# Kernel tuning notes

Measured on AMD Instinct MI355X. Metric: run time of the kernel, lower is better.

## Reference

```python
import jax, jax.numpy as jnp
import numpy as np

D_MODEL = 1024
D_FF = 4096


def _layernorm(x, g, b, eps=1e-5):
    mu = jnp.mean(x, axis=-1, keepdims=True)
    var = jnp.var(x, axis=-1, keepdims=True)
    return (x - mu) * jax.lax.rsqrt(var + eps) * g + b


def setup_inputs() -> dict:
    key = jax.random.key(0)
    ks = jax.random.split(key, 16)
    d, f = D_MODEL, D_FF
    s = 1.0 / np.sqrt(d)
    inp = {
        'x': jax.random.normal(ks[0], (4, 2048, d), dtype=jnp.float32),
        'wq': jax.random.uniform(ks[1], (d, d), jnp.float32, -s, s),
        'bq': jax.random.uniform(ks[2], (d,), jnp.float32, -s, s),
        'wk': jax.random.uniform(ks[3], (d, d), jnp.float32, -s, s),
        'bk': jax.random.uniform(ks[4], (d,), jnp.float32, -s, s),
        'wv': jax.random.uniform(ks[5], (d, d), jnp.float32, -s, s),
        'bv': jax.random.uniform(ks[6], (d,), jnp.float32, -s, s),
        'wo': jax.random.uniform(ks[7], (d, d), jnp.float32, -s, s),
        'bo': jax.random.uniform(ks[8], (d,), jnp.float32, -s, s),
        'w1': jax.random.uniform(ks[9], (d, f), jnp.float32, -s, s),
        'b1': jax.random.uniform(ks[10], (f,), jnp.float32, -s, s),
        'w2': jax.random.uniform(ks[11], (f, d), jnp.float32, -1.0 / np.sqrt(f), 1.0 / np.sqrt(f)),
        'b2': jax.random.uniform(ks[12], (d,), jnp.float32, -1.0 / np.sqrt(f), 1.0 / np.sqrt(f)),
        'g1': jnp.ones((d,), jnp.float32),
        'be1': jnp.zeros((d,), jnp.float32),
        'g2': jnp.ones((d,), jnp.float32),
        'be2': jnp.zeros((d,), jnp.float32),
    }
    return inp


def reference(x, wq, bq, wk, bk, wv, bv, wo, bo, w1, b1, w2, b2, g1, be1, g2, be2):
    d_k = x.shape[-1]
    q = jnp.einsum('bsd,de->bse', x, wq) + bq
    k = jnp.einsum('bsd,de->bse', x, wk) + bk
    v = jnp.einsum('bsd,de->bse', x, wv) + bv
    # full-width attention (no head split in the original module)
    scores = jnp.einsum('bqd,bkd->bqk', q, k) / jnp.sqrt(jnp.float32(d_k))
    attn = jax.nn.softmax(scores, axis=-1)
    ctx = jnp.einsum('bqk,bkd->bqd', attn, v)
    attn_out = jnp.einsum('bsd,de->bse', ctx, wo) + bo
    x1 = _layernorm(x + attn_out, g1, be1)
    ff = jnp.einsum('bsf,fd->bsd', jax.nn.relu(jnp.einsum('bsd,df->bsf', x1, w1) + b1), w2) + b2
    return _layernorm(x1 + ff, g2, be2)
```

## Files before the change

kernel.cpp:

```cpp
#include <hip/hip_runtime.h>
#include <stdint.h>


using f32x4 = __attribute__((ext_vector_type(4))) float;
using s16x8 = __attribute__((ext_vector_type(8))) short;

__device__ __forceinline__ ushort f2b(float f) {
    union { float f; uint32_t u; } v; v.f = f;
    uint32_t u = v.u;
    return (ushort)((u + 0x7fffu + ((u >> 16) & 1u)) >> 16);
}
__device__ __forceinline__ float b2f(ushort b) {
    union { uint32_t u; float f; } v; v.u = ((uint32_t)b) << 16;
    return v.f;
}
__device__ __forceinline__ float to_f(float f) { return f; }
__device__ __forceinline__ float to_f(ushort b) { return b2f(b); }

__device__ __forceinline__ void async_ld16(const ushort* g, ushort* l) {
    __builtin_amdgcn_global_load_lds(
        (const __attribute__((address_space(1))) void*)g,
        (__attribute__((address_space(3))) void*)l,
        16, 0, 0);
}

#define WAITCNT_VM4 0x0F74
#define WAITCNT_VM0 0x0F70


__global__ __launch_bounds__(256) void cast_f2b4(const float* __restrict__ src,
                                                 ushort* __restrict__ dst,
                                                 long long n4) {
    long long i = (long long)blockIdx.x * 256 + threadIdx.x;
    if (i >= n4) return;
    float4 f = ((const float4*)src)[i];
    ushort4 o;
    o.x = f2b(f.x); o.y = f2b(f.y); o.z = f2b(f.z); o.w = f2b(f.w);
    ((ushort4*)dst)[i] = o;
}


__global__ __launch_bounds__(256) void concat3(const float* __restrict__ a,
                                               const float* __restrict__ b,
                                               const float* __restrict__ c,
                                               float* __restrict__ dst) {
    int i = blockIdx.x * 256 + threadIdx.x;
    const float* s = (i < 1024) ? a : (i < 2048) ? b : c;
    dst[i] = s[i & 1023];
}


template <typename T>
__global__ __launch_bounds__(256) void transpose_to_bf16(const T* __restrict__ src,
                                                         ushort* __restrict__ dst,
                                                         int R, int C, int srcLd,
                                                         long long ss, long long ds) {
    __shared__ float tile[32][33];
    src += (long long)blockIdx.z * ss;
    dst += (long long)blockIdx.z * ds;
    const int c0 = blockIdx.x * 32;
    const int r0 = blockIdx.y * 32;
    const int tx = threadIdx.x, ty = threadIdx.y;
#pragma unroll
    for (int i = 0; i < 4; i++) {
        int r = r0 + ty + i * 8;
        tile[ty + i * 8][tx] = to_f(src[(long long)r * srcLd + c0 + tx]);
    }
    __syncthreads();
#pragma unroll
    for (int i = 0; i < 4; i++) {
        int r = c0 + ty + i * 8;
        dst[(long long)r * R + r0 + tx] = f2b(tile[tx][ty + i * 8]);
    }
}


__global__ __launch_bounds__(256) void transpose4_to_bf16(const float* __restrict__ s0,
                                                          const float* __restrict__ s1,
                                                          const float* __restrict__ s2,
                                                          const float* __restrict__ s3,
                                                          ushort* __restrict__ dst) {
    __shared__ float tile[32][33];
    const int D = 1024;
    const int z = blockIdx.z;
    const float* src = (z == 0) ? s0 : (z == 1) ? s1 : (z == 2) ? s2 : s3;
    dst += (long long)z * D * D;
    const int c0 = blockIdx.x * 32;
    const int r0 = blockIdx.y * 32;
    const int tx = threadIdx.x, ty = threadIdx.y;
#pragma unroll
    for (int i = 0; i < 4; i++) {
        int r = r0 + ty + i * 8;
        tile[ty + i * 8][tx] = src[(long long)r * D + c0 + tx];
    }
    __syncthreads();
#pragma unroll
    for (int i = 0; i < 4; i++) {
        int r = c0 + ty + i * 8;
        dst[(long long)r * D + r0 + tx] = f2b(tile[tx][ty + i * 8]);
    }
}


#define BM 128
#define BN 128
#define BKK 32
#define TILE_ELEMS (BM * BKK)

template <int OUT_BF16, int RELU, int HAS_BIAS>
__global__ __launch_bounds__(256, 4) void gemm_bt(const ushort* __restrict__ A,
                                                  const ushort* __restrict__ BT,
                                                  void* __restrict__ Cp,
                                                  const float* __restrict__ bias,
                                                  int N, int K, int kChunks, float scale,
                                                  int lda, int ldb, int ldc,
                                                  long long sA, long long sB, long long sC,
                                                  long long sK) {
    __shared__ ushort As[2 * TILE_ELEMS];
    __shared__ ushort Bs[2 * TILE_ELEMS];

    const int tid = threadIdx.x;
    const int kIdx = blockIdx.z % kChunks;
    const int bz = blockIdx.z / kChunks;
    const int kLen = K / kChunks;
    const int kOff = kIdx * kLen;
    const ushort* Ab = A + (long long)bz * sA;
    const ushort* Bb = BT + (long long)bz * sB;

    const int W = gridDim.x, H = gridDim.y;
    const int b = blockIdx.y * W + blockIdx.x;
    const int Hp = H >> 3;
    const int xcd = b & 7;
    const int s = b >> 3;
    const int tn = s / Hp;
    const int tm = xcd * Hp + (s % Hp);

    const int lane = tid & 63;
    const int wave = tid >> 6;
    const int wm = (wave >> 1) * 64;
    const int wn = (wave & 1) * 64;
    const int quad = lane >> 4;
    const int l16 = lane & 15;

    const int srow = wave * 32 + (lane >> 2);
    const int scol = (lane & 3) * 8;
    const ushort* AgL = Ab + (long long)(tm * BM + srow) * lda + scol + kOff;
    const ushort* BgL = Bb + (long long)(tn * BN + srow) * ldb + scol + kOff;
    ushort* AsL = As + wave * 1024;
    ushort* BsL = Bs + wave * 1024;
    const long long rstepA = (long long)16 * lda;
    const long long rstepB = (long long)16 * ldb;

    f32x4 acc[4][4];
#pragma unroll
    for (int i = 0; i < 4; i++)
#pragma unroll
        for (int j = 0; j < 4; j++) acc[i][j] = (f32x4){0.f, 0.f, 0.f, 0.f};

    async_ld16(AgL, AsL);
    async_ld16(AgL + rstepA, AsL + 512);
    async_ld16(BgL, BsL);
    async_ld16(BgL + rstepB, BsL + 512);

    int p = 0;
    for (int k0 = 0; k0 < kLen; k0 += BKK) {
        if (k0 + BKK < kLen) {
            const int q = p ^ 1;
            async_ld16(AgL + (k0 + BKK), AsL + q * TILE_ELEMS);
            async_ld16(AgL + rstepA + (k0 + BKK), AsL + q * TILE_ELEMS + 512);
            async_ld16(BgL + (k0 + BKK), BsL + q * TILE_ELEMS);
            async_ld16(BgL + rstepB + (k0 + BKK), BsL + q * TILE_ELEMS + 512);
            __builtin_amdgcn_s_waitcnt(WAITCNT_VM4);
        } else {
            __builtin_amdgcn_s_waitcnt(WAITCNT_VM0);
        }
        __builtin_amdgcn_s_barrier();

        const ushort* Asp = As + p * TILE_ELEMS;
        const ushort* Bsp = Bs + p * TILE_ELEMS;
        s16x8 af[4], bf[4];
#pragma unroll
        for (int i = 0; i < 4; i++)
            af[i] = *(const s16x8*)&Asp[(wm + i * 16 + l16) * BKK + quad * 8];
#pragma unroll
        for (int j = 0; j < 4; j++)
            bf[j] = *(const s16x8*)&Bsp[(wn + j * 16 + l16) * BKK + quad * 8];
#pragma unroll
        for (int i = 0; i < 4; i++)
#pragma unroll
            for (int j = 0; j < 4; j++)
                acc[i][j] = __builtin_amdgcn_mfma_f32_16x16x32_bf16(af[i], bf[j], acc[i][j], 0, 0, 0);

        __builtin_amdgcn_s_barrier();
        p ^= 1;
    }

    const long long cb = (long long)bz * sC + (long long)kIdx * sK;
    float* Cf = (float*)Cp;
    ushort* Cb = (ushort*)Cp;
#pragma unroll
    for (int j = 0; j < 4; j++) {
        const int col = tn * BN + wn + j * 16 + l16;
        float bv = (HAS_BIAS && kIdx == 0) ? bias[col] : 0.0f;
#pragma unroll
        for (int i = 0; i < 4; i++) {
            const int row0 = tm * BM + wm + i * 16 + quad * 4;
#pragma unroll
            for (int r = 0; r < 4; r++) {
                float v = acc[i][j][r] * scale + bv;
                if (RELU) v = v > 0.f ? v : 0.f;
                long long idx = cb + (long long)(row0 + r) * ldc + col;
                if (OUT_BF16) Cb[idx] = f2b(v);
                else Cf[idx] = v;
            }
        }
    }
}


__global__ __launch_bounds__(256) void softmax_rows(const ushort* __restrict__ S,
                                                    ushort* __restrict__ P) {
    const int C = 2048;
    const long long row = blockIdx.x;
    const int tid = threadIdx.x;
    const ushort4* s4 = (const ushort4*)(S + row * C) + tid * 2;
    ushort4 a = s4[0], bq = s4[1];
    float v[8];
    v[0] = b2f(a.x); v[1] = b2f(a.y); v[2] = b2f(a.z); v[3] = b2f(a.w);
    v[4] = b2f(bq.x); v[5] = b2f(bq.y); v[6] = b2f(bq.z); v[7] = b2f(bq.w);
    float mx = -1e30f;
#pragma unroll
    for (int i = 0; i < 8; i++) mx = fmaxf(mx, v[i]);
    __shared__ float red[256];
    red[tid] = mx;
    __syncthreads();
    for (int off = 128; off > 0; off >>= 1) {
        if (tid < off) red[tid] = fmaxf(red[tid], red[tid + off]);
        __syncthreads();
    }
    mx = red[0];
    __syncthreads();
    float sum = 0.f;
#pragma unroll
    for (int i = 0; i < 8; i++) {
        v[i] = __expf(v[i] - mx);
        sum += v[i];
    }
    red[tid] = sum;
    __syncthreads();
    for (int off = 128; off > 0; off >>= 1) {
        if (tid < off) red[tid] += red[tid + off];
        __syncthreads();
    }
    float inv = 1.f / red[0];
    ushort4 o0, o1;
    o0.x = f2b(v[0] * inv); o0.y = f2b(v[1] * inv); o0.z = f2b(v[2] * inv); o0.w = f2b(v[3] * inv);
    o1.x = f2b(v[4] * inv); o1.y = f2b(v[5] * inv); o1.z = f2b(v[6] * inv); o1.w = f2b(v[7] * inv);
    ushort4* p4 = (ushort4*)(P + row * C) + tid * 2;
    p4[0] = o0;
    p4[1] = o1;
}


__global__ __launch_bounds__(256) void residual_ln(const float* __restrict__ X,
                                                   const float* __restrict__ Y,
                                                   const float* __restrict__ Y2,
                                                   const float* __restrict__ g,
                                                   const float* __restrict__ be,
                                                   float* __restrict__ outf,
                                                   ushort* __restrict__ outb) {
    const int D = 1024;
    const long long row = blockIdx.x;
    const float* x = X + row * D;
    const float* y = Y + row * D;
    const float* y2 = Y2 ? Y2 + row * D : nullptr;
    const int tid = threadIdx.x;
    float v[4];
    float s = 0.f, s2 = 0.f;
#pragma unroll
    for (int i = 0; i < 4; i++) {
        int c = tid + i * 256;
        float t = x[c] + y[c];
        if (y2) t += y2[c];
        v[i] = t;
        s += t;
        s2 += t * t;
    }
    __shared__ float r1[256], r2[256];
    r1[tid] = s;
    r2[tid] = s2;
    __syncthreads();
    for (int off = 128; off > 0; off >>= 1) {
        if (tid < off) {
            r1[tid] += r1[tid + off];
            r2[tid] += r2[tid + off];
        }
        __syncthreads();
    }
    float mu = r1[0] * (1.f / 1024.f);
    float var = r2[0] * (1.f / 1024.f) - mu * mu;
    float inv = rsqrtf(var + 1e-5f);
    float* of = outf + row * D;
    ushort* ob = outb ? outb + row * D : nullptr;
#pragma unroll
    for (int i = 0; i < 4; i++) {
        int c = tid + i * 256;
        float o = (v[i] - mu) * inv * g[c] + be[c];
        of[c] = o;
        if (ob) ob[c] = f2b(o);
    }
}


extern "C" void kernel_launch(void* const* d_in, const int* in_sizes, int n_in,
                              void* d_out, int out_size, void* d_ws, size_t ws_size,
                              hipStream_t stream) {
    const float* x  = (const float*)d_in[0];
    const float* wq = (const float*)d_in[1];
    const float* bq = (const float*)d_in[2];
    const float* wk = (const float*)d_in[3];
    const float* bk = (const float*)d_in[4];
    const float* wv = (const float*)d_in[5];
    const float* bv = (const float*)d_in[6];
    const float* wo = (const float*)d_in[7];
    const float* bo = (const float*)d_in[8];
    const float* w1 = (const float*)d_in[9];
    const float* b1 = (const float*)d_in[10];
    const float* w2 = (const float*)d_in[11];
    const float* b2 = (const float*)d_in[12];
    const float* g1 = (const float*)d_in[13];
    const float* be1 = (const float*)d_in[14];
    const float* g2 = (const float*)d_in[15];
    const float* be2 = (const float*)d_in[16];
    float* out = (float*)d_out;
    char* ws = (char*)d_ws;

    const int Bz = 4, S = 2048, D = 1024, F = 4096;
    const int T = Bz * S;
    const size_t MBy = 1024ull * 1024ull;

    ushort* qkvT = (ushort*)(ws + 0);
    ushort* woT  = (ushort*)(ws + 6 * MBy);
    ushort* w1T  = (ushort*)(ws + 8 * MBy);
    ushort* w2T  = (ushort*)(ws + 16 * MBy);
    float*  bqkv = (float*)(ws + 24 * MBy);
    ushort* xb   = (ushort*)(ws + 25 * MBy);
    ushort* qkv  = (ushort*)(ws + 41 * MBy);
    ushort* vT   = (ushort*)(ws + 89 * MBy);
    ushort* scb  = (ushort*)(ws + 105 * MBy);
    ushort* attn = (ushort*)(ws + 169 * MBy);
    ushort* ctx = (ushort*)(ws + 25 * MBy);
    float*  ao0 = (float*)(ws + 105 * MBy);
    float*  ao1 = (float*)(ws + 137 * MBy);
    float*  x1  = (float*)(ws + 41 * MBy);
    ushort* x1b = (ushort*)(ws + 73 * MBy);
    ushort* h   = (ushort*)(ws + 105 * MBy);
    float*  ff0 = (float*)(ws + 169 * MBy);
    float*  ff1 = (float*)(ws + 73 * MBy);

    dim3 b32(32, 8);

    cast_f2b4<<<(T * D) / 1024, 256, 0, stream>>>(x, xb, (long long)(T * D) / 4);

    transpose4_to_bf16<<<dim3(32, 32, 4), b32, 0, stream>>>(wq, wk, wv, wo, qkvT);
    transpose_to_bf16<float><<<dim3(128, 32, 1), b32, 0, stream>>>(w1, w1T, D, F, F, 0, 0);
    transpose_to_bf16<float><<<dim3(32, 128, 1), b32, 0, stream>>>(w2, w2T, F, D, D, 0, 0);

    concat3<<<12, 256, 0, stream>>>(bq, bk, bv, bqkv);

    gemm_bt<1, 0, 1><<<dim3(3 * D / 128, T / 128, 1), 256, 0, stream>>>(
        xb, qkvT, qkv, bqkv, 3 * D, D, 1, 1.f, D, D, 3 * D, 0, 0, 0, 0);

    transpose_to_bf16<ushort><<<dim3(D / 32, S / 32, Bz), b32, 0, stream>>>(
        qkv + 2048, vT, S, D, 3 * D, (long long)S * 3 * D, (long long)S * D);

    gemm_bt<1, 0, 0><<<dim3(S / 128, S / 128, Bz), 256, 0, stream>>>(
        qkv, qkv + 1024, scb, nullptr, S, D, 1, 0.03125f, 3 * D, 3 * D, S,
        (long long)S * 3 * D, (long long)S * 3 * D, (long long)S * S, 0);

    softmax_rows<<<T, 256, 0, stream>>>(scb, attn);

    gemm_bt<1, 0, 0><<<dim3(D / 128, S / 128, Bz), 256, 0, stream>>>(
        attn, vT, ctx, nullptr, D, S, 1, 1.f, S, S, D,
        (long long)S * S, (long long)D * S, (long long)S * D, 0);

    gemm_bt<0, 0, 1><<<dim3(D / 128, T / 128, 2), 256, 0, stream>>>(
        ctx, woT, ao0, bo, D, D, 2, 1.f, D, D, D, 0, 0, 0, (long long)(ao1 - ao0));

    residual_ln<<<T, 256, 0, stream>>>(x, ao0, ao1, g1, be1, x1, x1b);

    gemm_bt<1, 1, 1><<<dim3(F / 128, T / 128, 1), 256, 0, stream>>>(
        x1b, w1T, h, b1, F, D, 1, 1.f, D, D, F, 0, 0, 0, 0);

    gemm_bt<0, 0, 1><<<dim3(D / 128, T / 128, 2), 256, 0, stream>>>(
        h, w2T, ff0, b2, D, F, 2, 1.f, F, F, D, 0, 0, 0, (long long)(ff1 - ff0));

    residual_ln<<<T, 256, 0, stream>>>(x1, ff0, ff1, g2, be2, out, nullptr);
}
```

Before: 596.0 us.

## Replace 128x128 GEMM with 256x256 8-wave swizzled pipelined GEMM kernel

Replaces the 128x128x32 bf16 MFMA GEMM with a 256x256x64 tile kernel using 512 threads. It uses XOR-swizzled LDS layouts, a staged half-tile async prefetch interleaved with four MFMA phases, and s_setprio around the MFMA blocks. The larger tile raises arithmetic intensity and cuts global traffic per flop. The attention-times-V GEMM is now split-K into two fp32 partials, followed by a new add-and-cast kernel that produces bf16 ctx. The costs are lower occupancy, fewer blocks on small grids (for example 4x8x8), and an extra pass over memory for ctx.

```diff
diff --git a/kernel.cpp b/kernel.cpp
--- a/kernel.cpp
+++ b/kernel.cpp
@@ -24,8 +24,9 @@
         16, 0, 0);
 }
 
-#define WAITCNT_VM4 0x0F74
-#define WAITCNT_VM0 0x0F70
+#define WAITCNT_VM6   0x0F76
+#define WAITCNT_VM0   0x0F70
+#define WAITCNT_LGKM0 0xC07F
 
 
 __global__ __launch_bounds__(256) void cast_f2b4(const float* __restrict__ src,
@@ -47,6 +48,21 @@
     int i = blockIdx.x * 256 + threadIdx.x;
     const float* s = (i < 1024) ? a : (i < 2048) ? b : c;
     dst[i] = s[i & 1023];
+}
+
+
+__global__ __launch_bounds__(256) void add2_cast(const float* __restrict__ a,
+                                                 const float* __restrict__ b,
+                                                 ushort* __restrict__ o,
+                                                 long long n4) {
+    long long i = (long long)blockIdx.x * 256 + threadIdx.x;
+    if (i >= n4) return;
+    float4 x = ((const float4*)a)[i];
+    float4 y = ((const float4*)b)[i];
+    ushort4 u;
+    u.x = f2b(x.x + y.x); u.y = f2b(x.y + y.y);
+    u.z = f2b(x.z + y.z); u.w = f2b(x.w + y.w);
+    ((ushort4*)o)[i] = u;
 }
 
 
@@ -102,109 +118,168 @@
 }
 
 
-#define BM 128
-#define BN 128
-#define BKK 32
-#define TILE_ELEMS (BM * BKK)
-
 template <int OUT_BF16, int RELU, int HAS_BIAS>
-__global__ __launch_bounds__(256, 4) void gemm_bt(const ushort* __restrict__ A,
+__global__ __launch_bounds__(512, 2) void gemm256(const ushort* __restrict__ A,
                                                   const ushort* __restrict__ BT,
                                                   void* __restrict__ Cp,
                                                   const float* __restrict__ bias,
-                                                  int N, int K, int kChunks, float scale,
+                                                  int K, int kChunks, float scale,
                                                   int lda, int ldb, int ldc,
-                                                  long long sA, long long sB, long long sC,
-                                                  long long sK) {
-    __shared__ ushort As[2 * TILE_ELEMS];
-    __shared__ ushort Bs[2 * TILE_ELEMS];
+                                                  long long sA, long long sB,
+                                                  long long sC, long long sK) {
+    __shared__ ushort Asl[32768];
+    __shared__ ushort Bsl[32768];
 
     const int tid = threadIdx.x;
     const int kIdx = blockIdx.z % kChunks;
     const int bz = blockIdx.z / kChunks;
     const int kLen = K / kChunks;
     const int kOff = kIdx * kLen;
+    const int kTiles = kLen >> 6;
     const ushort* Ab = A + (long long)bz * sA;
     const ushort* Bb = BT + (long long)bz * sB;
 
     const int W = gridDim.x, H = gridDim.y;
-    const int b = blockIdx.y * W + blockIdx.x;
+    const int bidx = blockIdx.y * W + blockIdx.x;
     const int Hp = H >> 3;
-    const int xcd = b & 7;
-    const int s = b >> 3;
-    const int tn = s / Hp;
-    const int tm = xcd * Hp + (s % Hp);
+    const int xcd = bidx & 7;
+    const int sb = bidx >> 3;
+    const int tn = sb / Hp;
+    const int tm = xcd * Hp + sb % Hp;
 
     const int lane = tid & 63;
-    const int wave = tid >> 6;
-    const int wm = (wave >> 1) * 64;
-    const int wn = (wave & 1) * 64;
+    const int w = tid >> 6;
+    const int wm = w >> 2;
+    const int wn = w & 3;
+    const int l16 = lane & 15;
     const int quad = lane >> 4;
-    const int l16 = lane & 15;
-
-    const int srow = wave * 32 + (lane >> 2);
-    const int scol = (lane & 3) * 8;
-    const ushort* AgL = Ab + (long long)(tm * BM + srow) * lda + scol + kOff;
-    const ushort* BgL = Bb + (long long)(tn * BN + srow) * ldb + scol + kOff;
-    ushort* AsL = As + wave * 1024;
-    ushort* BsL = Bs + wave * 1024;
-    const long long rstepA = (long long)16 * lda;
-    const long long rstepB = (long long)16 * ldb;
-
-    f32x4 acc[4][4];
-#pragma unroll
-    for (int i = 0; i < 4; i++)
+
+    const int lr = lane >> 3;
+    const int swslot = (lane & 7) ^ lr;
+    const ushort* AgS = Ab + (long long)(tm * 256 + w * 16 + lr) * lda + kOff + swslot * 8;
+    const ushort* BgS = Bb + (long long)(tn * 256 + w * 16 + lr) * ldb + kOff + swslot * 8;
+    ushort* AsW = Asl + w * 1024;
+    ushort* BsW = Bsl + w * 1024;
+
+#define STG_A(h, tt, bf) { const ushort* g_ = AgS + (h) * 128 * lda + (tt) * 64;   \
+        ushort* d_ = AsW + (bf) * 16384 + (h) * 8192;                              \
+        async_ld16(g_, d_); async_ld16(g_ + 8 * lda, d_ + 512); }
+#define STG_B(h, tt, bf) { const ushort* g_ = BgS + (h) * 128 * ldb + (tt) * 64;   \
+        ushort* d_ = BsW + (bf) * 16384 + (h) * 8192;                              \
+        async_ld16(g_, d_); async_ld16(g_ + 8 * ldb, d_ + 512); }
+
+    const int csw0 = (quad * 8) ^ ((l16 & 7) * 8);
+    const int csw1 = (32 + quad * 8) ^ ((l16 & 7) * 8);
+    const int aoff0 = l16 * 64 + csw0;
+    const int aoff1 = l16 * 64 + csw1;
+    const ushort* AhB = Asl + wm * 8192;
+    const ushort* BhB = Bsl + (wn >> 1) * 8192 + (wn & 1) * 4096;
+
+    f32x4 acc[8][4];
+#pragma unroll
+    for (int i = 0; i < 8; i++)
 #pragma unroll
         for (int j = 0; j < 4; j++) acc[i][j] = (f32x4){0.f, 0.f, 0.f, 0.f};
 
-    async_ld16(AgL, AsL);
-    async_ld16(AgL + rstepA, AsL + 512);
-    async_ld16(BgL, BsL);
-    async_ld16(BgL + rstepB, BsL + 512);
+    STG_B(0, 0, 0); STG_A(0, 0, 0); STG_B(1, 0, 0); STG_A(1, 0, 0);
+    STG_B(0, 1, 1); STG_A(0, 1, 1); STG_B(1, 1, 1);
+    __builtin_amdgcn_s_waitcnt(WAITCNT_VM6);
+    __builtin_amdgcn_s_barrier();
 
     int p = 0;
-    for (int k0 = 0; k0 < kLen; k0 += BKK) {
-        if (k0 + BKK < kLen) {
-            const int q = p ^ 1;
-            async_ld16(AgL + (k0 + BKK), AsL + q * TILE_ELEMS);
-            async_ld16(AgL + rstepA + (k0 + BKK), AsL + q * TILE_ELEMS + 512);
-            async_ld16(BgL + (k0 + BKK), BsL + q * TILE_ELEMS);
-            async_ld16(BgL + rstepB + (k0 + BKK), BsL + q * TILE_ELEMS + 512);
-            __builtin_amdgcn_s_waitcnt(WAITCNT_VM4);
-        } else {
-            __builtin_amdgcn_s_waitcnt(WAITCNT_VM0);
+    for (int t = 0; t < kTiles; ++t, p ^= 1) {
+        const ushort* Ap = AhB + p * 16384;
+        const ushort* Bp = BhB + p * 16384;
+        s16x8 a0[4][2], a1[4][2], bb[4][2];
+
+#pragma unroll
+        for (int i = 0; i < 4; i++) {
+            a0[i][0] = *(const s16x8*)(Ap + i * 1024 + aoff0);
+            a0[i][1] = *(const s16x8*)(Ap + i * 1024 + aoff1);
         }
-        __builtin_amdgcn_s_barrier();
-
-        const ushort* Asp = As + p * TILE_ELEMS;
-        const ushort* Bsp = Bs + p * TILE_ELEMS;
-        s16x8 af[4], bf[4];
-#pragma unroll
-        for (int i = 0; i < 4; i++)
-            af[i] = *(const s16x8*)&Asp[(wm + i * 16 + l16) * BKK + quad * 8];
-#pragma unroll
-        for (int j = 0; j < 4; j++)
-            bf[j] = *(const s16x8*)&Bsp[(wn + j * 16 + l16) * BKK + quad * 8];
-#pragma unroll
-        for (int i = 0; i < 4; i++)
-#pragma unroll
-            for (int j = 0; j < 4; j++)
-                acc[i][j] = __builtin_amdgcn_mfma_f32_16x16x32_bf16(af[i], bf[j], acc[i][j], 0, 0, 0);
-
-        __builtin_amdgcn_s_barrier();
-        p ^= 1;
-    }
+#pragma unroll
+        for (int j = 0; j < 4; j++) {
+            bb[j][0] = *(const s16x8*)(Bp + j * 1024 + aoff0);
+            bb[j][1] = *(const s16x8*)(Bp + j * 1024 + aoff1);
+        }
+        if (t + 1 < kTiles) STG_A(1, t + 1, p ^ 1);
+        __builtin_amdgcn_s_barrier();
+        __builtin_amdgcn_s_waitcnt(WAITCNT_LGKM0);
+        __builtin_amdgcn_s_setprio(1);
+#pragma unroll
+        for (int ks = 0; ks < 2; ks++)
+#pragma unroll
+            for (int i = 0; i < 4; i++)
+#pragma unroll
+                for (int j = 0; j < 2; j++)
+                    acc[i][j] = __builtin_amdgcn_mfma_f32_16x16x32_bf16(
+                        a0[i][ks], bb[j][ks], acc[i][j], 0, 0, 0);
+        __builtin_amdgcn_s_setprio(0);
+        __builtin_amdgcn_s_barrier();
+
+#pragma unroll
+        for (int i = 0; i < 4; i++) {
+            a1[i][0] = *(const s16x8*)(Ap + 4096 + i * 1024 + aoff0);
+            a1[i][1] = *(const s16x8*)(Ap + 4096 + i * 1024 + aoff1);
+        }
+        if (t + 2 < kTiles) STG_B(0, t + 2, p);
+        __builtin_amdgcn_s_barrier();
+        __builtin_amdgcn_s_setprio(1);
+#pragma unroll
+        for (int ks = 0; ks < 2; ks++)
+#pragma unroll
+            for (int i = 0; i < 4; i++)
+#pragma unroll
+                for (int j = 0; j < 2; j++)
+                    acc[i][2 + j] = __builtin_amdgcn_mfma_f32_16x16x32_bf16(
+                        a0[i][ks], bb[2 + j][ks], acc[i][2 + j], 0, 0, 0);
+        __builtin_amdgcn_s_setprio(0);
+        __builtin_amdgcn_s_barrier();
+
+        if (t + 2 < kTiles) STG_A(0, t + 2, p);
+        __builtin_amdgcn_s_barrier();
+        __builtin_amdgcn_s_waitcnt(WAITCNT_LGKM0);
+        __builtin_amdgcn_s_setprio(1);
+#pragma unroll
+        for (int ks = 0; ks < 2; ks++)
+#pragma unroll
+            for (int i = 0; i < 4; i++)
+#pragma unroll
+                for (int j = 0; j < 2; j++)
+                    acc[4 + i][j] = __builtin_amdgcn_mfma_f32_16x16x32_bf16(
+                        a1[i][ks], bb[j][ks], acc[4 + i][j], 0, 0, 0);
+        __builtin_amdgcn_s_setprio(0);
+        __builtin_amdgcn_s_barrier();
+
+        if (t + 2 < kTiles) STG_B(1, t + 2, p);
+        __builtin_amdgcn_s_barrier();
+        __builtin_amdgcn_s_setprio(1);
+#pragma unroll
+        for (int ks = 0; ks < 2; ks++)
+#pragma unroll
+            for (int i = 0; i < 4; i++)
+#pragma unroll
+                for (int j = 0; j < 2; j++)
+                    acc[4 + i][2 + j] = __builtin_amdgcn_mfma_f32_16x16x32_bf16(
+                        a1[i][ks], bb[2 + j][ks], acc[4 + i][2 + j], 0, 0, 0);
+        __builtin_amdgcn_s_setprio(0);
+        if (t + 2 < kTiles) __builtin_amdgcn_s_waitcnt(WAITCNT_VM6);
+        else if (t + 1 < kTiles) __builtin_amdgcn_s_waitcnt(WAITCNT_VM0);
+        __builtin_amdgcn_s_barrier();
+    }
+#undef STG_A
+#undef STG_B
 
     const long long cb = (long long)bz * sC + (long long)kIdx * sK;
     float* Cf = (float*)Cp;
     ushort* Cb = (ushort*)Cp;
 #pragma unroll
     for (int j = 0; j < 4; j++) {
-        const int col = tn * BN + wn + j * 16 + l16;
+        const int col = tn * 256 + wn * 64 + j * 16 + l16;
         float bv = (HAS_BIAS && kIdx == 0) ? bias[col] : 0.0f;
 #pragma unroll
-        for (int i = 0; i < 4; i++) {
-            const int row0 = tm * BM + wm + i * 16 + quad * 4;
+        for (int i = 0; i < 8; i++) {
+            const int row0 = tm * 256 + wm * 128 + i * 16 + quad * 4;
 #pragma unroll
             for (int r = 0; r < 4; r++) {
                 float v = acc[i][j][r] * scale + bv;
@@ -349,7 +424,9 @@
     ushort* vT   = (ushort*)(ws + 89 * MBy);
     ushort* scb  = (ushort*)(ws + 105 * MBy);
     ushort* attn = (ushort*)(ws + 169 * MBy);
-    ushort* ctx = (ushort*)(ws + 25 * MBy);
+    float*  ctx0 = (float*)(ws + 105 * MBy);
+    float*  ctx1 = (float*)(ws + 137 * MBy);
+    ushort* ctxb = (ushort*)(ws + 25 * MBy);
     float*  ao0 = (float*)(ws + 105 * MBy);
     float*  ao1 = (float*)(ws + 137 * MBy);
     float*  x1  = (float*)(ws + 41 * MBy);
@@ -368,32 +445,34 @@
 
     concat3<<<12, 256, 0, stream>>>(bq, bk, bv, bqkv);
 
-    gemm_bt<1, 0, 1><<<dim3(3 * D / 128, T / 128, 1), 256, 0, stream>>>(
-        xb, qkvT, qkv, bqkv, 3 * D, D, 1, 1.f, D, D, 3 * D, 0, 0, 0, 0);
+    gemm256<1, 0, 1><<<dim3(3 * D / 256, T / 256, 1), 512, 0, stream>>>(
+        xb, qkvT, qkv, bqkv, D, 1, 1.f, D, D, 3 * D, 0, 0, 0, 0);
 
     transpose_to_bf16<ushort><<<dim3(D / 32, S / 32, Bz), b32, 0, stream>>>(
         qkv + 2048, vT, S, D, 3 * D, (long long)S * 3 * D, (long long)S * D);
 
-    gemm_bt<1, 0, 0><<<dim3(S / 128, S / 128, Bz), 256, 0, stream>>>(
-        qkv, qkv + 1024, scb, nullptr, S, D, 1, 0.03125f, 3 * D, 3 * D, S,
+    gemm256<1, 0, 0><<<dim3(S / 256, S / 256, Bz), 512, 0, stream>>>(
+        qkv, qkv + 1024, scb, nullptr, D, 1, 0.03125f, 3 * D, 3 * D, S,
         (long long)S * 3 * D, (long long)S * 3 * D, (long long)S * S, 0);
 
     softmax_rows<<<T, 256, 0, stream>>>(scb, attn);
 
-    gemm_bt<1, 0, 0><<<dim3(D / 128, S / 128, Bz), 256, 0, stream>>>(
-        attn, vT, ctx, nullptr, D, S, 1, 1.f, S, S, D,
-        (long long)S * S, (long long)D * S, (long long)S * D, 0);
-
-    gemm_bt<0, 0, 1><<<dim3(D / 128, T / 128, 2), 256, 0, stream>>>(
-        ctx, woT, ao0, bo, D, D, 2, 1.f, D, D, D, 0, 0, 0, (long long)(ao1 - ao0));
+    gemm256<0, 0, 0><<<dim3(D / 256, S / 256, Bz * 2), 512, 0, stream>>>(
+        attn, vT, ctx0, nullptr, S, 2, 1.f, S, S, D,
+        (long long)S * S, (long long)D * S, (long long)S * D, (long long)(ctx1 - ctx0));
+
+    add2_cast<<<(T * D) / 1024, 256, 0, stream>>>(ctx0, ctx1, ctxb, (long long)(T * D) / 4);
+
+    gemm256<0, 0, 1><<<dim3(D / 256, T / 256, 2), 512, 0, stream>>>(
+        ctxb, woT, ao0, bo, D, 2, 1.f, D, D, D, 0, 0, 0, (long long)(ao1 - ao0));
 
     residual_ln<<<T, 256, 0, stream>>>(x, ao0, ao1, g1, be1, x1, x1b);
 
-    gemm_bt<1, 1, 1><<<dim3(F / 128, T / 128, 1), 256, 0, stream>>>(
-        x1b, w1T, h, b1, F, D, 1, 1.f, D, D, F, 0, 0, 0, 0);
-
-    gemm_bt<0, 0, 1><<<dim3(D / 128, T / 128, 2), 256, 0, stream>>>(
-        h, w2T, ff0, b2, D, F, 2, 1.f, F, F, D, 0, 0, 0, (long long)(ff1 - ff0));
+    gemm256<1, 1, 1><<<dim3(F / 256, T / 256, 1), 512, 0, stream>>>(
+        x1b, w1T, h, b1, D, 1, 1.f, D, D, F, 0, 0, 0, 0);
+
+    gemm256<0, 0, 1><<<dim3(D / 256, T / 256, 2), 512, 0, stream>>>(
+        h, w2T, ff0, b2, F, 2, 1.f, F, F, D, 0, 0, 0, (long long)(ff1 - ff0));
 
     residual_ln<<<T, 256, 0, stream>>>(x1, ff0, ff1, g2, be2, out, nullptr);
 }
```

After: 601.6 us. About the same (+0.9%).
